# Optimization experiments

Measured on AMD Instinct MI355X. Metric: run time of the kernel, lower is better.

Reference implementation:

```python
import jax, jax.numpy as jnp
import numpy as np

# The TF layer iterates index in range(0,60,3) and j in range(index+3,63,3),
# computing for each ordered pair (i<k) of the 21 landmarks the unit-ish
# direction components clip((p_k - p_i)/||p_k - p_i||, -1, 1), appending
# (x_tilt, y_tilt) per pair. All slices use indices < 63, so despite the
# repeated concatenation the source vectors always come from the original
# 63 input columns. Output = concat([input, 2*210 pair features]) -> [B,483].

_PAIRS_I, _PAIRS_K = [], []
for _i in range(20):
    for _k in range(_i + 1, 21):
        _PAIRS_I.append(_i)
        _PAIRS_K.append(_k)
_PAIRS_I = np.array(_PAIRS_I, dtype=np.int32)  # (210,)
_PAIRS_K = np.array(_PAIRS_K, dtype=np.int32)  # (210,)


def setup_inputs() -> dict:
    key = jax.random.key(0)
    tensor = jax.random.normal(key, (500000, 63), dtype=jnp.float32)
    return {"tensor": tensor}


def reference(tensor) -> jnp.ndarray:
    B = tensor.shape[0]
    # (x, y) of each of the 21 landmarks; original layout is [x,y,z]*21
    pts = tensor[:, :63].reshape(B, 21, 3)[:, :, :2]          # [B, 21, 2]
    vec = pts[:, _PAIRS_K] - pts[:, _PAIRS_I]                  # [B, 210, 2]
    norms = jnp.linalg.norm(vec, axis=-1, keepdims=True)       # [B, 210, 1]
    tilts = jnp.clip(vec / norms, -1.0, 1.0)                   # [B, 210, 2]
    out = jnp.concatenate([tensor, tilts.reshape(B, 420)], axis=-1)  # [B, 483]
    return out.astype(jnp.float32)
```

## Files before the change

### kernel.cpp

```cpp
#include <hip/hip_runtime.h>
#include <math.h>


#define ROWS 16
#define NCOLS 63
#define OUTCOLS 483
#define NPAIRS 210
#define BLOCK 256

__global__ __launch_bounds__(BLOCK) void angular_kernel(
    const float* __restrict__ in, float* __restrict__ out, int B) {
    __shared__ float s_in[ROWS * NCOLS];
    __shared__ float s_out[ROWS * OUTCOLS];
    __shared__ int   s_pi[NPAIRS];
    __shared__ int   s_pk[NPAIRS];

    const int t = threadIdx.x;

    if (t < NPAIRS) {
        int p = t, i = 0, off = 0;
        while (off + (20 - i) <= p) { off += 20 - i; ++i; }
        s_pi[t] = 3 * i;
        s_pk[t] = 3 * (i + 1 + (p - off));
    }

    const size_t row0 = (size_t)blockIdx.x * ROWS;
    const bool full = (row0 + ROWS) <= (size_t)B;

    if (full) {
        const float4* gin4 = (const float4*)(in + row0 * NCOLS);
        float4* s_in4 = (float4*)s_in;
        if (t < (ROWS * NCOLS) / 4) s_in4[t] = gin4[t];
    } else {
        for (int idx = t; idx < ROWS * NCOLS; idx += BLOCK) {
            size_t g = row0 * NCOLS + (size_t)idx;
            if (g < (size_t)B * NCOLS) s_in[idx] = in[g];
        }
    }
    __syncthreads();

    const int r = t >> 4;
    const int l = t & 15;
    const float* rowin  = s_in  + r * NCOLS;
    float*       rowout = s_out + r * OUTCOLS;

    for (int c = l; c < NCOLS; c += 16) rowout[c] = rowin[c];

    for (int p = l; p < NPAIRS; p += 16) {
        const int ia = s_pi[p], ka = s_pk[p];
        const float vx = rowin[ka]     - rowin[ia];
        const float vy = rowin[ka + 1] - rowin[ia + 1];
        const float inv = rsqrtf(vx * vx + vy * vy);
        float tx = vx * inv;
        float ty = vy * inv;
        tx = fminf(fmaxf(tx, -1.0f), 1.0f);
        ty = fminf(fmaxf(ty, -1.0f), 1.0f);
        rowout[NCOLS + 2 * p]     = tx;
        rowout[NCOLS + 2 * p + 1] = ty;
    }
    __syncthreads();

    if (full) {
        float4* gout4 = (float4*)(out + row0 * OUTCOLS);
        const float4* s_out4 = (const float4*)s_out;
        for (int idx = t; idx < (ROWS * OUTCOLS) / 4; idx += BLOCK)
            gout4[idx] = s_out4[idx];
    } else {
        for (int idx = t; idx < ROWS * OUTCOLS; idx += BLOCK) {
            size_t g = row0 * OUTCOLS + (size_t)idx;
            if (g < (size_t)B * OUTCOLS) out[g] = s_out[idx];
        }
    }
}

extern "C" void kernel_launch(void* const* d_in, const int* in_sizes, int n_in,
                              void* d_out, int out_size, void* d_ws, size_t ws_size,
                              hipStream_t stream) {
    const float* in = (const float*)d_in[0];
    float* out = (float*)d_out;
    const int B = in_sizes[0] / NCOLS;
    const int grid = (B + ROWS - 1) / ROWS;
    hipLaunchKernelGGL(angular_kernel, dim3(grid), dim3(BLOCK), 0, stream, in, out, B);
}
```

Baseline: 1.011 ms.

## Use persistent slab kernel with double-buffered input and compile-time pair unrolling

Replaces the one-block-per-16-rows kernel with a persistent grid of 256 blocks of 1024 threads. Each block walks 64-row slabs and prefetches the next slab's input into a second shared buffer while computing the current one. Each wave handles a fixed range of pairs with compile-time indices, unrolled through template recursion, with the row's landmarks held in registers instead of read through shared-memory index tables. The cost is about 140KB of dynamic shared memory, so only one block fits per CU, and the grid may underfill the device. A fallback to the old kernel is kept in case the shared-memory attribute cannot be set.

```diff
diff --git a/kernel.cpp b/kernel.cpp
--- a/kernel.cpp
+++ b/kernel.cpp
@@ -2,71 +2,202 @@
 #include <math.h>
 
 
-#define ROWS 16
-#define NCOLS 63
-#define OUTCOLS 483
-#define NPAIRS 210
-#define BLOCK 256
-
-__global__ __launch_bounds__(BLOCK) void angular_kernel(
+#define NCOLS    63
+#define OUTCOLS  483
+#define NPAIRS   210
+#define SROWS    64
+#define BLOCK    1024
+#define GRIDB    256
+
+#define IN_SLAB_F4   ((SROWS * NCOLS) / 4)
+#define OUT_SLAB_F   (SROWS * OUTCOLS)
+#define SMEM_FLOATS  (OUT_SLAB_F + 2 * SROWS * NCOLS)
+
+constexpr int pair_i(int p) {
+    int i = 0, off = 0;
+    while (off + (20 - i) <= p) { off += 20 - i; ++i; }
+    return i;
+}
+constexpr int pair_k(int p) {
+    int i = 0, off = 0;
+    while (off + (20 - i) <= p) { off += 20 - i; ++i; }
+    return i + 1 + (p - off);
+}
+
+template<int P, int PEND>
+struct PairChain {
+    static __device__ __forceinline__ void run(const float (&lm)[42],
+                                               float* __restrict__ rowout) {
+        constexpr int i = pair_i(P);
+        constexpr int k = pair_k(P);
+        const float vx = lm[2 * k]     - lm[2 * i];
+        const float vy = lm[2 * k + 1] - lm[2 * i + 1];
+        const float inv = rsqrtf(vx * vx + vy * vy);
+        float tx = fminf(fmaxf(vx * inv, -1.0f), 1.0f);
+        float ty = fminf(fmaxf(vy * inv, -1.0f), 1.0f);
+        rowout[NCOLS + 2 * P]     = tx;
+        rowout[NCOLS + 2 * P + 1] = ty;
+        PairChain<P + 1, PEND>::run(lm, rowout);
+    }
+};
+template<int PEND>
+struct PairChain<PEND, PEND> {
+    static __device__ __forceinline__ void run(const float (&)[42],
+                                               float* __restrict__) {}
+};
+
+template<int W>
+__device__ __forceinline__ void wave_compute(const float* __restrict__ rowin,
+                                             float* __restrict__ rowout) {
+    constexpr int C0 = 4 * W;
+    constexpr int C1 = (4 * W + 4 < NCOLS) ? (4 * W + 4) : NCOLS;
+#pragma unroll
+    for (int c = C0; c < C1; ++c) rowout[c] = rowin[c];
+
+    float lm[42];
+#pragma unroll
+    for (int i = 0; i < 21; ++i) {
+        lm[2 * i]     = rowin[3 * i];
+        lm[2 * i + 1] = rowin[3 * i + 1];
+    }
+    constexpr int P0 = (W < 2) ? 14 * W : 28 + 13 * (W - 2);
+    constexpr int P1 = (W < 2) ? P0 + 14 : P0 + 13;
+    PairChain<P0, P1>::run(lm, rowout);
+}
+
+__global__ __launch_bounds__(BLOCK) void angular_slab_kernel(
+    const float* __restrict__ in, float* __restrict__ out, int B, int nslab) {
+    extern __shared__ float smem[];
+    float* s_out = smem;
+    float* s_inA = smem + OUT_SLAB_F;
+    float* s_inB = s_inA + SROWS * NCOLS;
+
+    const int t = threadIdx.x;
+    const int w = t >> 6;
+    const int l = t & 63;
+    const size_t total_in4 = ((size_t)B * NCOLS) >> 2;
+    const float4* __restrict__ gin4 = (const float4*)in;
+
+    const size_t slab0 = blockIdx.x;
+    if (t < IN_SLAB_F4) {
+        const size_t g = slab0 * IN_SLAB_F4 + (size_t)t;
+        float4 r = make_float4(0.f, 0.f, 0.f, 0.f);
+        if (g < total_in4) r = gin4[g];
+        ((float4*)s_inA)[t] = r;
+    }
+    __syncthreads();
+
+    int cur = 0;
+    for (size_t slab = slab0; slab < (size_t)nslab; slab += gridDim.x) {
+        const size_t nxt = slab + gridDim.x;
+        const bool havenxt = nxt < (size_t)nslab;
+        float4 r = make_float4(0.f, 0.f, 0.f, 0.f);
+        if (havenxt && t < IN_SLAB_F4) {
+            const size_t g = nxt * IN_SLAB_F4 + (size_t)t;
+            if (g < total_in4) r = gin4[g];
+        }
+
+        {
+            const float* __restrict__ s_cur = cur ? s_inB : s_inA;
+            const float* __restrict__ rowin = s_cur + l * NCOLS;
+            float* __restrict__ rowout = s_out + l * OUTCOLS;
+            switch (w) {
+                case 0:  wave_compute<0>(rowin, rowout);  break;
+                case 1:  wave_compute<1>(rowin, rowout);  break;
+                case 2:  wave_compute<2>(rowin, rowout);  break;
+                case 3:  wave_compute<3>(rowin, rowout);  break;
+                case 4:  wave_compute<4>(rowin, rowout);  break;
+                case 5:  wave_compute<5>(rowin, rowout);  break;
+                case 6:  wave_compute<6>(rowin, rowout);  break;
+                case 7:  wave_compute<7>(rowin, rowout);  break;
+                case 8:  wave_compute<8>(rowin, rowout);  break;
+                case 9:  wave_compute<9>(rowin, rowout);  break;
+                case 10: wave_compute<10>(rowin, rowout); break;
+                case 11: wave_compute<11>(rowin, rowout); break;
+                case 12: wave_compute<12>(rowin, rowout); break;
+                case 13: wave_compute<13>(rowin, rowout); break;
+                case 14: wave_compute<14>(rowin, rowout); break;
+                default: wave_compute<15>(rowin, rowout); break;
+            }
+        }
+        __syncthreads();
+
+        {
+            const size_t row0 = slab * SROWS;
+            const size_t rows = ((size_t)B - row0 >= SROWS) ? SROWS
+                                                            : ((size_t)B - row0);
+            float4* __restrict__ gout4 = (float4*)(out + row0 * OUTCOLS);
+            const float4* s_out4 = (const float4*)s_out;
+            const int lim4 = (int)((rows * OUTCOLS) >> 2);
+            for (int idx = t; idx < lim4; idx += BLOCK)
+                gout4[idx] = s_out4[idx];
+            const int rem = (int)((rows * OUTCOLS) & 3);
+            if (rem && t < rem)
+                out[row0 * OUTCOLS + (size_t)lim4 * 4 + t] = s_out[lim4 * 4 + t];
+        }
+
+        if (havenxt && t < IN_SLAB_F4) {
+            float* s_nxt = cur ? s_inA : s_inB;
+            ((float4*)s_nxt)[t] = r;
+        }
+        __syncthreads();
+        cur ^= 1;
+    }
+}
+
+#define FROWS 16
+#define FBLOCK 256
+
+__global__ __launch_bounds__(FBLOCK) void angular_kernel_small(
     const float* __restrict__ in, float* __restrict__ out, int B) {
-    __shared__ float s_in[ROWS * NCOLS];
-    __shared__ float s_out[ROWS * OUTCOLS];
+    __shared__ float s_in[FROWS * NCOLS];
+    __shared__ float s_out[FROWS * OUTCOLS];
     __shared__ int   s_pi[NPAIRS];
     __shared__ int   s_pk[NPAIRS];
 
     const int t = threadIdx.x;
-
     if (t < NPAIRS) {
         int p = t, i = 0, off = 0;
         while (off + (20 - i) <= p) { off += 20 - i; ++i; }
         s_pi[t] = 3 * i;
         s_pk[t] = 3 * (i + 1 + (p - off));
     }
-
-    const size_t row0 = (size_t)blockIdx.x * ROWS;
-    const bool full = (row0 + ROWS) <= (size_t)B;
-
+    const size_t row0 = (size_t)blockIdx.x * FROWS;
+    const bool full = (row0 + FROWS) <= (size_t)B;
     if (full) {
         const float4* gin4 = (const float4*)(in + row0 * NCOLS);
         float4* s_in4 = (float4*)s_in;
-        if (t < (ROWS * NCOLS) / 4) s_in4[t] = gin4[t];
+        if (t < (FROWS * NCOLS) / 4) s_in4[t] = gin4[t];
     } else {
-        for (int idx = t; idx < ROWS * NCOLS; idx += BLOCK) {
+        for (int idx = t; idx < FROWS * NCOLS; idx += FBLOCK) {
             size_t g = row0 * NCOLS + (size_t)idx;
             if (g < (size_t)B * NCOLS) s_in[idx] = in[g];
         }
     }
     __syncthreads();
-
     const int r = t >> 4;
     const int l = t & 15;
     const float* rowin  = s_in  + r * NCOLS;
     float*       rowout = s_out + r * OUTCOLS;
-
     for (int c = l; c < NCOLS; c += 16) rowout[c] = rowin[c];
-
     for (int p = l; p < NPAIRS; p += 16) {
         const int ia = s_pi[p], ka = s_pk[p];
         const float vx = rowin[ka]     - rowin[ia];
         const float vy = rowin[ka + 1] - rowin[ia + 1];
         const float inv = rsqrtf(vx * vx + vy * vy);
-        float tx = vx * inv;
-        float ty = vy * inv;
-        tx = fminf(fmaxf(tx, -1.0f), 1.0f);
-        ty = fminf(fmaxf(ty, -1.0f), 1.0f);
+        float tx = fminf(fmaxf(vx * inv, -1.0f), 1.0f);
+        float ty = fminf(fmaxf(vy * inv, -1.0f), 1.0f);
         rowout[NCOLS + 2 * p]     = tx;
         rowout[NCOLS + 2 * p + 1] = ty;
     }
     __syncthreads();
-
     if (full) {
         float4* gout4 = (float4*)(out + row0 * OUTCOLS);
         const float4* s_out4 = (const float4*)s_out;
-        for (int idx = t; idx < (ROWS * OUTCOLS) / 4; idx += BLOCK)
+        for (int idx = t; idx < (FROWS * OUTCOLS) / 4; idx += FBLOCK)
             gout4[idx] = s_out4[idx];
     } else {
-        for (int idx = t; idx < ROWS * OUTCOLS; idx += BLOCK) {
+        for (int idx = t; idx < FROWS * OUTCOLS; idx += FBLOCK) {
             size_t g = row0 * OUTCOLS + (size_t)idx;
             if (g < (size_t)B * OUTCOLS) out[g] = s_out[idx];
         }
@@ -79,6 +210,25 @@
     const float* in = (const float*)d_in[0];
     float* out = (float*)d_out;
     const int B = in_sizes[0] / NCOLS;
-    const int grid = (B + ROWS - 1) / ROWS;
-    hipLaunchKernelGGL(angular_kernel, dim3(grid), dim3(BLOCK), 0, stream, in, out, B);
-}
+    const int nslab = (B + SROWS - 1) / SROWS;
+
+    static int use_big = -1;
+    if (use_big < 0) {
+        hipError_t e = hipFuncSetAttribute(
+            reinterpret_cast<const void*>(&angular_slab_kernel),
+            hipFuncAttributeMaxDynamicSharedMemorySize,
+            (int)(SMEM_FLOATS * sizeof(float)));
+        use_big = (e == hipSuccess) ? 1 : 0;
+    }
+
+    if (use_big) {
+        int grid = GRIDB;
+        if (grid > nslab) grid = nslab;
+        hipLaunchKernelGGL(angular_slab_kernel, dim3(grid), dim3(BLOCK),
+                           SMEM_FLOATS * sizeof(float), stream, in, out, B, nslab);
+    } else {
+        const int grid = (B + FROWS - 1) / FROWS;
+        hipLaunchKernelGGL(angular_kernel_small, dim3(grid), dim3(FBLOCK), 0,
+                           stream, in, out, B);
+    }
+}
```

Result: no change. 1.026 ms (+1.5%).

## Compute output float4 chunks directly from shared input, drop output staging

Applied to the files above, without the earlier changes.

The kernel no longer stages the 483-column output rows in shared memory. Each thread now computes four consecutive output floats straight from the shared input slab and writes them as one float4 to global memory. This removes the large shared output buffer, which should help occupancy, and removes the second barrier. The cost is redundant work: each pair's rsqrt is computed twice (once for x, once for y), plus per-element index division and branching. Rows per block go from 16 to 32, and the pair table is packed into a single int.

```diff
diff --git a/kernel.cpp b/kernel.cpp
--- a/kernel.cpp
+++ b/kernel.cpp
@@ -2,74 +2,104 @@
 #include <math.h>
 
 
-#define ROWS 16
-#define NCOLS 63
-#define OUTCOLS 483
-#define NPAIRS 210
-#define BLOCK 256
+#define NCOLS    63
+#define OUTCOLS  483
+#define NPAIRS   210
+#define ROWS     32
+#define BLOCK    256
 
-__global__ __launch_bounds__(BLOCK) void angular_kernel(
+#define IN_SLAB   (ROWS * NCOLS)
+#define IN_SLAB4  (IN_SLAB / 4)
+
+__global__ __launch_bounds__(BLOCK) void angular_direct_kernel(
     const float* __restrict__ in, float* __restrict__ out, int B) {
-    __shared__ float s_in[ROWS * NCOLS];
-    __shared__ float s_out[ROWS * OUTCOLS];
-    __shared__ int   s_pi[NPAIRS];
-    __shared__ int   s_pk[NPAIRS];
+    __shared__ float s_in[IN_SLAB];
+    __shared__ int   s_tab[NPAIRS];
 
     const int t = threadIdx.x;
 
     if (t < NPAIRS) {
         int p = t, i = 0, off = 0;
-        while (off + (20 - i) <= p) { off += 20 - i; ++i; }
-        s_pi[t] = 3 * i;
-        s_pk[t] = 3 * (i + 1 + (p - off));
+#pragma unroll 1
+        for (int it = 0; it < 20; ++it) {
+            if (off + (20 - i) <= p) { off += 20 - i; ++i; } else break;
+        }
+        int k = i + 1 + (p - off);
+        s_tab[t] = (3 * k << 16) | (3 * i);
     }
 
     const size_t row0 = (size_t)blockIdx.x * ROWS;
-    const bool full = (row0 + ROWS) <= (size_t)B;
+    if (row0 >= (size_t)B) return;
+    const int rows = ((size_t)B - row0 >= ROWS) ? ROWS : (int)((size_t)B - row0);
 
-    if (full) {
-        const float4* gin4 = (const float4*)(in + row0 * NCOLS);
-        float4* s_in4 = (float4*)s_in;
-        if (t < (ROWS * NCOLS) / 4) s_in4[t] = gin4[t];
+    if (rows == ROWS) {
+        const float4* __restrict__ gin4 = (const float4*)(in + row0 * NCOLS);
+        float4* s4 = (float4*)s_in;
+#pragma unroll
+        for (int j = 0; j < (IN_SLAB4 + BLOCK - 1) / BLOCK; ++j) {
+            const int idx = t + j * BLOCK;
+            if (idx < IN_SLAB4) s4[idx] = gin4[idx];
+        }
     } else {
-        for (int idx = t; idx < ROWS * NCOLS; idx += BLOCK) {
-            size_t g = row0 * NCOLS + (size_t)idx;
-            if (g < (size_t)B * NCOLS) s_in[idx] = in[g];
-        }
+        for (int idx = t; idx < rows * NCOLS; idx += BLOCK)
+            s_in[idx] = in[row0 * NCOLS + (size_t)idx];
     }
     __syncthreads();
 
-    const int r = t >> 4;
-    const int l = t & 15;
-    const float* rowin  = s_in  + r * NCOLS;
-    float*       rowout = s_out + r * OUTCOLS;
+    const int nfloat = rows * OUTCOLS;
+    const int nchunk = nfloat >> 2;
+    float4* __restrict__ gout4 = (float4*)(out + row0 * OUTCOLS);
 
-    for (int c = l; c < NCOLS; c += 16) rowout[c] = rowin[c];
+    for (int q = t; q < nchunk; q += BLOCK) {
+        const int f0 = q << 2;
+        const int r0 = f0 / OUTCOLS;
+        const int c0 = f0 - r0 * OUTCOLS;
+        float vals[4];
+#pragma unroll
+        for (int u = 0; u < 4; ++u) {
+            int r = r0, c = c0 + u;
+            if (c >= OUTCOLS) { ++r; c -= OUTCOLS; }
+            const float* __restrict__ rowin = s_in + r * NCOLS;
+            float v;
+            if (c < NCOLS) {
+                v = rowin[c];
+            } else {
+                const int idx = c - NCOLS;
+                const int tab = s_tab[idx >> 1];
+                const int ia = tab & 0xffff;
+                const int ka = tab >> 16;
+                const float vx = rowin[ka]     - rowin[ia];
+                const float vy = rowin[ka + 1] - rowin[ia + 1];
+                const float inv = rsqrtf(vx * vx + vy * vy);
+                const float tv = ((idx & 1) ? vy : vx) * inv;
+                v = fminf(fmaxf(tv, -1.0f), 1.0f);
+            }
+            vals[u] = v;
+        }
+        gout4[q] = make_float4(vals[0], vals[1], vals[2], vals[3]);
+    }
 
-    for (int p = l; p < NPAIRS; p += 16) {
-        const int ia = s_pi[p], ka = s_pk[p];
-        const float vx = rowin[ka]     - rowin[ia];
-        const float vy = rowin[ka + 1] - rowin[ia + 1];
-        const float inv = rsqrtf(vx * vx + vy * vy);
-        float tx = vx * inv;
-        float ty = vy * inv;
-        tx = fminf(fmaxf(tx, -1.0f), 1.0f);
-        ty = fminf(fmaxf(ty, -1.0f), 1.0f);
-        rowout[NCOLS + 2 * p]     = tx;
-        rowout[NCOLS + 2 * p + 1] = ty;
-    }
-    __syncthreads();
-
-    if (full) {
-        float4* gout4 = (float4*)(out + row0 * OUTCOLS);
-        const float4* s_out4 = (const float4*)s_out;
-        for (int idx = t; idx < (ROWS * OUTCOLS) / 4; idx += BLOCK)
-            gout4[idx] = s_out4[idx];
-    } else {
-        for (int idx = t; idx < ROWS * OUTCOLS; idx += BLOCK) {
-            size_t g = row0 * OUTCOLS + (size_t)idx;
-            if (g < (size_t)B * OUTCOLS) out[g] = s_out[idx];
+    const int rem = nfloat & 3;
+    if (rem && t < rem) {
+        const int fi = (nchunk << 2) + t;
+        const int r = fi / OUTCOLS;
+        const int c = fi - r * OUTCOLS;
+        const float* __restrict__ rowin = s_in + r * NCOLS;
+        float v;
+        if (c < NCOLS) {
+            v = rowin[c];
+        } else {
+            const int idx = c - NCOLS;
+            const int tab = s_tab[idx >> 1];
+            const int ia = tab & 0xffff;
+            const int ka = tab >> 16;
+            const float vx = rowin[ka]     - rowin[ia];
+            const float vy = rowin[ka + 1] - rowin[ia + 1];
+            const float inv = rsqrtf(vx * vx + vy * vy);
+            const float tv = ((idx & 1) ? vy : vx) * inv;
+            v = fminf(fmaxf(tv, -1.0f), 1.0f);
         }
+        out[row0 * OUTCOLS + (size_t)fi] = v;
     }
 }
 
@@ -79,6 +109,8 @@
     const float* in = (const float*)d_in[0];
     float* out = (float*)d_out;
     const int B = in_sizes[0] / NCOLS;
+    if (B <= 0) return;
     const int grid = (B + ROWS - 1) / ROWS;
-    hipLaunchKernelGGL(angular_kernel, dim3(grid), dim3(BLOCK), 0, stream, in, out, B);
+    hipLaunchKernelGGL(angular_direct_kernel, dim3(grid), dim3(BLOCK), 0,
+                       stream, in, out, B);
 }
```

New measurement: 1.019 ms. Within noise of the previous version (+0.8%).
